# Kernel optimization log

Hardware: AMD Instinct MI355X
Metric: run time of the kernel (lower is better)

## Reference

```python
import jax, jax.numpy as jnp
import numpy as np

B, S, D = 1, 2048, 1024
F = 1408            # expert intermediate dim
E = 16              # num experts
K = 2               # top_k
CAP_FACTOR = 1.25


def _mlp(h, wg, wu, wd):
    # DeepSeek-style gated MLP (SwiGLU, no bias)
    return (jax.nn.silu(h @ wg) * (h @ wu)) @ wd


def setup_inputs() -> dict:
    key = jax.random.key(0)
    ks = jax.random.split(key, 10)
    sd = 0.02
    return {
        "x": jax.random.normal(ks[0], (B, S, D), jnp.float32),
        "router_w": jax.random.normal(ks[1], (D, E), jnp.float32) * sd,
        "router_b": jnp.zeros((E,), jnp.float32),
        "w_gate": jax.random.normal(ks[2], (E, D, F), jnp.float32) * sd,
        "w_up": jax.random.normal(ks[3], (E, D, F), jnp.float32) * sd,
        "w_down": jax.random.normal(ks[4], (E, F, D), jnp.float32) * sd,
        "sw_gate": jax.random.normal(ks[5], (D, F), jnp.float32) * sd,
        "sw_up": jax.random.normal(ks[6], (D, F), jnp.float32) * sd,
        "sw_down": jax.random.normal(ks[7], (F, D), jnp.float32) * sd,
    }


def reference(x, router_w, router_b, w_gate, w_up, w_down, sw_gate, sw_up, sw_down):
    b, s, d = x.shape
    N = b * s
    NK = N * K
    C = int(np.ceil(CAP_FACTOR * NK / E))  # per-expert capacity

    x_tokens = x.reshape(N, d)

    # Router: softmax -> top-k -> renormalize
    logits = x_tokens @ router_w + router_b           # [N, E]
    probs = jax.nn.softmax(logits, axis=-1)
    vals, idx = jax.lax.top_k(probs, K)               # [N, K]
    vals = vals / (jnp.sum(vals, axis=-1, keepdims=True) + 1e-9)
    idx_flat = idx.reshape(NK)                        # int expert ids
    vals_flat = vals.reshape(NK)

    # Position within each expert's buffer = rank in flattened (token, k) order.
    # Same math as (cumsum(one_hot)*one_hot).sum(-1)-1 in the original.
    oh_e = jax.nn.one_hot(idx_flat, E, dtype=x.dtype)             # [NK, E] (small)
    pos = (jnp.cumsum(oh_e, axis=0) * oh_e).sum(axis=1) - 1       # [NK]
    within = (pos < C).astype(x.dtype)                            # capacity mask
    pos_c = jnp.clip(pos, 0, C - 1).astype(jnp.int32)

    # Dispatch: scatter tokens into per-expert buffers. Positions are unique
    # per expert, so scatter-add equals the dense one-hot einsum exactly.
    token_ids = jnp.arange(NK) // K
    x_pair = x_tokens[token_ids] * within[:, None]                # [NK, D]
    expert_inputs = jnp.zeros((E, C, d), x.dtype).at[idx_flat, pos_c].add(x_pair)

    # Grouped expert MLPs
    expert_outputs = jax.vmap(_mlp)(expert_inputs, w_gate, w_up, w_down)  # [E, C, D]

    # Combine: gather back and weight by renormalized router probs
    gathered = expert_outputs[idx_flat, pos_c] * (vals_flat * within)[:, None]
    output_tokens = gathered.reshape(N, K, d).sum(axis=1)         # [N, D]

    return x + _mlp(x, sw_gate, sw_up, sw_down) + output_tokens.reshape(b, s, d)
```

## Files before the change

### kernel.cpp

```cpp
#include <hip/hip_runtime.h>
#include <hip/hip_bf16.h>

#define TOKENS 2048
#define DIM    1024
#define FDIM   1408
#define NEXP   16
#define NK     (TOKENS * 2)
#define CAP    320
#define RPAD   384

typedef __attribute__((ext_vector_type(4))) float f32x4;
typedef __attribute__((ext_vector_type(2))) float f32x2;
typedef __attribute__((ext_vector_type(8))) short s16x8;
typedef __attribute__((ext_vector_type(4))) short s16x4;

__device__ __forceinline__ short f2bf(float f) {
    unsigned int u = __float_as_uint(f);
    u += 0x7FFFu + ((u >> 16) & 1u);
    return (short)(u >> 16);
}
__device__ __forceinline__ float bf2f(short s) {
    return __uint_as_float(((unsigned int)(unsigned short)s) << 16);
}
__device__ __forceinline__ unsigned int f2bf_pk(float lo, float hi) {
    union { __hip_bfloat162 h; unsigned int u; } c;
    c.h = __float22bfloat162_rn(make_float2(lo, hi));
    return c.u;
}

#define GLDS16(gp, lp) __builtin_amdgcn_global_load_lds(                     \
    (const __attribute__((address_space(1))) unsigned int*)(gp),             \
    (__attribute__((address_space(3))) unsigned int*)(lp), 16, 0, 0)

struct GSegF {
    const short* A; long aStride; int aRpad;
    const float* B0; const float* B1; long bStride;
    short* Out; long oStride; int oRpad;
    const int* cnt; int Mb, Nb, N, K, nblocks;
};
struct GSegB {
    const short* A; long aStride; int aRpad;
    const short* B0; long bStride;
    short* Out; long oStride;
    const int* cnt; int Mb, Nb, N, K, nblocks;
};
struct WSeg { const float* in; short* out; int K, N, mats, nblocks; };

__device__ void wchunk_dev(const WSeg& W, int bid)
{
    const int spm = W.K >> 3;
    const int mat = bid / spm, s = bid % spm;
    const float* in  = W.in  + (size_t)mat * W.K * W.N + (size_t)s * 8 * W.N;
    short* out = W.out + (size_t)mat * W.K * W.N + (size_t)s * W.N * 8;
    const int t = threadIdx.x;
    const int iters = (W.N + 511) >> 9;
    for (int it = 0; it < iters; it++) {
        const int n = it * 512 + 2 * t;
        if (n >= W.N) break;
        const float* src = in + n;
        s16x8 o0, o1;
#pragma unroll
        for (int j = 0; j < 8; j++) {
            float2 v = *(const float2*)(src + (size_t)j * W.N);
            o0[j] = f2bf(v.x);
            o1[j] = f2bf(v.y);
        }
        *(s16x8*)(out + (size_t)n * 8)     = o0;
        *(s16x8*)(out + (size_t)n * 8 + 8) = o1;
    }
}

__device__ void router_dev(const float* __restrict__ x, const float* __restrict__ rw,
                           const float* __restrict__ rb, int* __restrict__ idx_flat,
                           float* __restrict__ vals_flat, int bid)
{
    __shared__ float lg[16][17];
    const int t  = threadIdx.x;
    const int tl = t >> 4;
    const int e  = t & 15;
    const int token = bid * 16 + tl;
    const float* xr = x + (size_t)token * DIM;

    float acc = 0.f;
    for (int d4 = 0; d4 < DIM / 4; d4++) {
        float4 xv = *(const float4*)(xr + d4 * 4);
        acc += xv.x * rw[(d4 * 4 + 0) * NEXP + e];
        acc += xv.y * rw[(d4 * 4 + 1) * NEXP + e];
        acc += xv.z * rw[(d4 * 4 + 2) * NEXP + e];
        acc += xv.w * rw[(d4 * 4 + 3) * NEXP + e];
    }
    lg[tl][e] = acc + rb[e];
    __syncthreads();

    if (t < 16) {
        float l[16];
#pragma unroll
        for (int j = 0; j < 16; j++) l[j] = lg[t][j];
        float m = l[0];
#pragma unroll
        for (int j = 1; j < 16; j++) m = fmaxf(m, l[j]);
        float p[16], den = 0.f;
#pragma unroll
        for (int j = 0; j < 16; j++) { p[j] = __expf(l[j] - m); den += p[j]; }
        int i1 = -1; float b1 = -1e30f;
#pragma unroll
        for (int j = 0; j < 16; j++) if (p[j] > b1) { b1 = p[j]; i1 = j; }
        int i2 = -1; float b2 = -1e30f;
#pragma unroll
        for (int j = 0; j < 16; j++) if (j != i1 && p[j] > b2) { b2 = p[j]; i2 = j; }
        float v1 = b1 / den, v2 = b2 / den;
        float s = v1 + v2 + 1e-9f;
        int tok = bid * 16 + t;
        idx_flat[tok * 2 + 0] = i1;
        idx_flat[tok * 2 + 1] = i2;
        vals_flat[tok * 2 + 0] = v1 / s;
        vals_flat[tok * 2 + 1] = v2 / s;
    }
}

__device__ void xconv_dev(const float* __restrict__ x, short* __restrict__ xb, int bid)
{
    const int token = bid * 2 + (threadIdx.x >> 7);
    const int c = threadIdx.x & 127;
    const float* src = x + (size_t)token * DIM + c * 8;
    float4 v0 = *(const float4*)(src);
    float4 v1 = *(const float4*)(src + 4);
    s16x8 o;
    o[0] = f2bf(v0.x); o[1] = f2bf(v0.y); o[2] = f2bf(v0.z); o[3] = f2bf(v0.w);
    o[4] = f2bf(v1.x); o[5] = f2bf(v1.y); o[6] = f2bf(v1.z); o[7] = f2bf(v1.w);
    *(s16x8*)(xb + (size_t)c * (TOKENS * 8) + (size_t)token * 8) = o;
}

__global__ __launch_bounds__(256) void rx_kernel(
    const float* __restrict__ x, const float* __restrict__ rw,
    const float* __restrict__ rb, int* __restrict__ idx_flat,
    float* __restrict__ vals, short* __restrict__ xb)
{
    int bid = blockIdx.x;
    if (bid < TOKENS / 16) { router_dev(x, rw, rb, idx_flat, vals, bid); return; }
    xconv_dev(x, xb, bid - TOKENS / 16);
}

__global__ void scan_kernel(const int* __restrict__ idx_flat,
                            const float* __restrict__ vals,
                            int* __restrict__ dst, float* __restrict__ wgt,
                            int* __restrict__ cnt)
{
    const int lane = threadIdx.x;
    int base[16];
#pragma unroll
    for (int e = 0; e < 16; e++) base[e] = 0;

    for (int c = 0; c < NK / 64; c++) {
        int i = c * 64 + lane;
        int e = idx_flat[i];
        unsigned long long m[16];
#pragma unroll
        for (int ee = 0; ee < 16; ee++) m[ee] = __ballot(e == ee);
        unsigned long long mym = 0ULL; int myb = 0;
#pragma unroll
        for (int ee = 0; ee < 16; ee++) {
            bool sel = (e == ee);
            mym = sel ? m[ee] : mym;
            myb = sel ? base[ee] : myb;
        }
        int pos = myb + (int)__popcll(mym & ((1ULL << lane) - 1ULL));
        bool within = pos < CAP;
        dst[i] = within ? (e * RPAD + pos) : -1;
        wgt[i] = within ? vals[i] : 0.f;
#pragma unroll
        for (int ee = 0; ee < 16; ee++) base[ee] += (int)__popcll(m[ee]);
    }
    if (lane < 16) cnt[lane] = base[lane] < CAP ? base[lane] : CAP;
}

__global__ __launch_bounds__(256) void scatter_kernel(
    const float* __restrict__ x, const int* __restrict__ dst,
    const int* __restrict__ idx_flat, short* __restrict__ ex)
{
    const int i = blockIdx.x * 2 + (threadIdx.x >> 7);
    const int d0 = dst[i];
    if (d0 < 0) return;
    const int e = idx_flat[i];
    const int pos = d0 - e * RPAD;
    const int token = i >> 1;
    const int c = threadIdx.x & 127;
    const float* src = x + (size_t)token * DIM + c * 8;
    float4 v0 = *(const float4*)(src);
    float4 v1 = *(const float4*)(src + 4);
    s16x8 o;
    o[0] = f2bf(v0.x); o[1] = f2bf(v0.y); o[2] = f2bf(v0.z); o[3] = f2bf(v0.w);
    o[4] = f2bf(v1.x); o[5] = f2bf(v1.y); o[6] = f2bf(v1.z); o[7] = f2bf(v1.w);
    *(s16x8*)(ex + (size_t)e * (DIM * RPAD) + (size_t)c * (RPAD * 8) +
              (size_t)pos * 8) = o;
}

template <int NMAT>
__device__ void gemm_fused_dev(const GSegF& S, int bid)
{
    constexpr int BUFS = 4096 * (1 + NMAT);
    __shared__ short lds[2 * BUFS];

    const int cpx = S.nblocks >> 3;
    const int lid = (bid & 7) * cpx + (bid >> 3);
    const int mb  = lid % S.Mb;
    const int t1  = lid / S.Mb;
    const int nb  = t1 % S.Nb;
    const int g   = t1 / S.Nb;
    const int m0 = mb * 128, n0 = nb * 128;
    if (S.cnt != nullptr && m0 >= S.cnt[g]) return;

    const int tid = threadIdx.x, lane = tid & 63, w = tid >> 6;
    const int wr = w >> 1, wc = w & 1, ln = lane & 15, kg = lane >> 4;
    const int N = S.N, K = S.K;

    const short* Ag  = S.A  + (size_t)g * S.aStride + (size_t)m0 * 8;
    const float* Bg0 = S.B0 + (size_t)g * S.bStride + n0;
    const float* Bg1 = nullptr;
    if constexpr (NMAT == 2) Bg1 = S.B1 + (size_t)g * S.bStride + n0;

    const size_t aR8 = (size_t)S.aRpad * 8;

    const int srow = tid & 127, sslab = tid >> 7;
    const short* aS0 = Ag + sslab * aR8 + srow * 8;
    const short* aS1 = Ag + (2 + sslab) * aR8 + srow * 8;
    const int dA0 = w * 512, dA1 = 2048 + w * 512;

    const float* bSrc;
    int rB, cW;
    if constexpr (NMAT == 2) {
        const int c4 = tid & 31, gq = (tid >> 5) & 3, mat = tid >> 7;
        bSrc = (mat ? Bg1 : Bg0) + (size_t)gq * 8 * N + c4 * 4;
        rB = 4096 + mat * 4096 + gq * 1024;
        cW = c4;
    } else {
        const int c2 = tid & 63, gq = tid >> 6;
        bSrc = Bg0 + (size_t)gq * 8 * N + c2 * 2;
        rB = 4096 + gq * 1024;
        cW = c2;
    }

    f32x4 bq[8];
    f32x2 bd[8];

    auto LOADB = [&](int ks) {
        const float* p = bSrc + (size_t)ks * 32 * N;
        if constexpr (NMAT == 2) {
#pragma unroll
            for (int j = 0; j < 8; j++) bq[j] = *(const f32x4*)(p + (size_t)j * N);
        } else {
#pragma unroll
            for (int j = 0; j < 8; j++) bd[j] = *(const f32x2*)(p + (size_t)j * N);
        }
    };
    auto STGA = [&](int buf, int ks) {
        const size_t ka = (size_t)ks * 4 * aR8;
        short* base = lds + buf * BUFS;
        GLDS16(aS0 + ka, base + dA0);
        GLDS16(aS1 + ka, base + dA1);
    };
    auto WRITEB = [&](int buf) {
        short* d = lds + buf * BUFS + rB;
        if constexpr (NMAT == 2) {
#pragma unroll
            for (int j = 0; j < 4; j++) {
                const int colS = (cW * 4 + j) ^ ((cW >> 1) & 7);
                uint4 o;
                o.x = f2bf_pk(bq[0][j], bq[1][j]);
                o.y = f2bf_pk(bq[2][j], bq[3][j]);
                o.z = f2bf_pk(bq[4][j], bq[5][j]);
                o.w = f2bf_pk(bq[6][j], bq[7][j]);
                *(uint4*)(d + colS * 8) = o;
            }
        } else {
#pragma unroll
            for (int j = 0; j < 2; j++) {
                const int colS = (cW * 2 + j) ^ ((cW >> 2) & 7);
                uint4 o;
                o.x = f2bf_pk(bd[0][j], bd[1][j]);
                o.y = f2bf_pk(bd[2][j], bd[3][j]);
                o.z = f2bf_pk(bd[4][j], bd[5][j]);
                o.w = f2bf_pk(bd[6][j], bd[7][j]);
                *(uint4*)(d + colS * 8) = o;
            }
        }
    };

    const int aO = kg * 1024 + (wr * 64 + ln) * 8;

    f32x4 acc[NMAT][4][4] = {};
    const int nt = K / 32;

    LOADB(0);
    __builtin_amdgcn_sched_barrier(0);
    STGA(0, 0);
    __builtin_amdgcn_sched_barrier(0);
    WRITEB(0);
    __builtin_amdgcn_sched_barrier(0);
    LOADB(1);
    __builtin_amdgcn_sched_barrier(0);
    asm volatile("s_waitcnt lgkmcnt(0)" ::: "memory");
    STGA(1, 1);
    __builtin_amdgcn_sched_barrier(0);

    int cur = 0;
    for (int ks = 0; ks < nt; ks++) {
        if (ks + 1 < nt) asm volatile("s_waitcnt vmcnt(10)" ::: "memory");
        else             asm volatile("s_waitcnt vmcnt(0)"  ::: "memory");
        __builtin_amdgcn_s_barrier();
        __builtin_amdgcn_sched_barrier(0);

        const short* base = lds + cur * BUFS;
        s16x8 af[4];
#pragma unroll
        for (int m = 0; m < 4; m++)
            af[m] = *(const s16x8*)(base + aO + m * 128);
        s16x8 bf[NMAT][4];
#pragma unroll
        for (int nf = 0; nf < 4; nf++) {
            const int col  = wc * 64 + nf * 16 + ln;
            const int colS = col ^ ((col >> 3) & 7);
#pragma unroll
            for (int mat = 0; mat < NMAT; mat++)
                bf[mat][nf] = *(const s16x8*)(base + 4096 + mat * 4096 +
                                              kg * 1024 + colS * 8);
        }

#pragma unroll
        for (int nf = 0; nf < 4; nf++)
#pragma unroll
            for (int m = 0; m < 4; m++)
#pragma unroll
                for (int mat = 0; mat < NMAT; mat++)
                    acc[mat][m][nf] = __builtin_amdgcn_mfma_f32_16x16x32_bf16(
                        af[m], bf[mat][nf], acc[mat][m][nf], 0, 0, 0);

        if (ks + 1 < nt) WRITEB(cur ^ 1);

        __builtin_amdgcn_sched_barrier(0);
        if (ks + 2 < nt) LOADB(ks + 2);
        __builtin_amdgcn_sched_barrier(0);
        asm volatile("s_waitcnt lgkmcnt(0)" ::: "memory");
        __builtin_amdgcn_s_barrier();

        if (ks + 2 < nt) {
            STGA(cur, ks + 2);
            __builtin_amdgcn_sched_barrier(0);
        }
        cur ^= 1;
    }

#pragma unroll
    for (int m = 0; m < 4; m++) {
#pragma unroll
        for (int nf = 0; nf < 4; nf++) {
            const int row = m0 + wr * 64 + m * 16 + kg * 4;
            const int col = n0 + wc * 64 + nf * 16 + ln;
#pragma unroll
            for (int j = 0; j < 4; j++) {
                if constexpr (NMAT == 2) {
                    float gv = acc[0][m][nf][j];
                    float uv = acc[1][m][nf][j];
                    float v = gv / (1.f + __expf(-gv)) * uv;
                    S.Out[(size_t)g * S.oStride + (size_t)(col >> 3) * (S.oRpad * 8) +
                          (size_t)(row + j) * 8 + (col & 7)] = f2bf(v);
                } else {
                    S.Out[(size_t)g * S.oStride + (size_t)(row + j) * N + col] =
                        f2bf(acc[0][m][nf][j]);
                }
            }
        }
    }
}

__device__ void gemm_down_dev(const GSegB& S, int bid)
{
    constexpr int BUFS = 10240;
    __shared__ short lds[2 * BUFS];

    const int cpx = S.nblocks >> 3;
    const int lid = (bid & 7) * cpx + (bid >> 3);
    const int mb  = lid % S.Mb;
    const int t1  = lid / S.Mb;
    const int nb  = t1 % S.Nb;
    const int g   = t1 / S.Nb;
    const int m0 = mb * 64, n0 = nb * 256;
    if (S.cnt != nullptr && m0 >= S.cnt[g]) return;

    const int tid = threadIdx.x, lane = tid & 63, w = tid >> 6;
    const int wr = w >> 1, wc = w & 1, ln = lane & 15, kg = lane >> 4;
    const int N = S.N, K = S.K;

    const short* Ag = S.A  + (size_t)g * S.aStride + (size_t)m0 * 8;
    const short* Bg = S.B0 + (size_t)g * S.bStride + (size_t)n0 * 8;

    const size_t aR8 = (size_t)S.aRpad * 8;
    const size_t n8  = (size_t)N * 8;

    const short* aS = Ag + (size_t)(tid >> 6) * aR8 + (size_t)(tid & 63) * 8;
    const short* bS = Bg + (size_t)tid * 8;
    const int dA = w * 512;

    auto STG = [&](int buf, int ks) {
        const size_t ka = (size_t)ks * 4 * aR8;
        const size_t kb = (size_t)ks * 4 * n8;
        short* base = lds + buf * BUFS;
        GLDS16(aS + ka, base + dA);
#pragma unroll
        for (int i = 0; i < 4; i++)
            GLDS16(bS + kb + (size_t)i * n8, base + 2048 + i * 2048 + w * 512);
    };

    const int aO = kg * 512 + (wr * 32 + ln) * 8;
    const int bBase = 2048 + kg * 2048 + (wc * 128 + ln) * 8;

    f32x4 acc[2][8] = {};
    const int nt = K / 32;
    STG(0, 0); STG(1, 1);
    int cur = 0;
    for (int ks = 0; ks < nt; ks++) {
        if (ks + 1 < nt) asm volatile("s_waitcnt vmcnt(5)" ::: "memory");
        else             asm volatile("s_waitcnt vmcnt(0)" ::: "memory");
        __builtin_amdgcn_s_barrier();
        __builtin_amdgcn_sched_barrier(0);

        const short* base = lds + cur * BUFS;
        s16x8 af[2];
        af[0] = *(const s16x8*)(base + aO);
        af[1] = *(const s16x8*)(base + aO + 128);
        s16x8 bf[8];
#pragma unroll
        for (int nf = 0; nf < 8; nf++)
            bf[nf] = *(const s16x8*)(base + bBase + nf * 128);

#pragma unroll
        for (int nf = 0; nf < 8; nf++)
#pragma unroll
            for (int m = 0; m < 2; m++)
                acc[m][nf] = __builtin_amdgcn_mfma_f32_16x16x32_bf16(
                    af[m], bf[nf], acc[m][nf], 0, 0, 0);

        __builtin_amdgcn_sched_barrier(0);
        __builtin_amdgcn_s_barrier();
        if (ks + 2 < nt) STG(cur, ks + 2);
        cur ^= 1;
    }

#pragma unroll
    for (int m = 0; m < 2; m++) {
#pragma unroll
        for (int nf = 0; nf < 8; nf++) {
            const int row = m0 + wr * 32 + m * 16 + kg * 4;
            const int col = n0 + wc * 128 + nf * 16 + ln;
#pragma unroll
            for (int j = 0; j < 4; j++)
                S.Out[(size_t)g * S.oStride + (size_t)(row + j) * N + col] =
                    f2bf(acc[m][nf][j]);
        }
    }
}

__global__ __launch_bounds__(256, 2) void gateup_kernel(GSegF s0, GSegF s1,
                                                        WSeg w0, WSeg w1)
{
    int bid = blockIdx.x;
    if (bid < s0.nblocks) { gemm_fused_dev<2>(s0, bid); return; }
    bid -= s0.nblocks;
    if (bid < s1.nblocks) { gemm_fused_dev<2>(s1, bid); return; }
    bid -= s1.nblocks;
    if (bid < w0.nblocks) { wchunk_dev(w0, bid); return; }
    wchunk_dev(w1, bid - w0.nblocks);
}

__global__ __launch_bounds__(256, 3) void down_kernel(GSegB s0, GSegB s1)
{
    int bid = blockIdx.x;
    if (bid < s0.nblocks) { gemm_down_dev(s0, bid); return; }
    gemm_down_dev(s1, bid - s0.nblocks);
}

__global__ __launch_bounds__(256) void combine_kernel(
    const float* __restrict__ x, const short* __restrict__ shout,
    const short* __restrict__ eout, const int* __restrict__ dst,
    const float* __restrict__ wgt, float* __restrict__ out)
{
    const int t = blockIdx.x;
    const int d = threadIdx.x * 4;
    size_t o = (size_t)t * DIM + d;
    float4 xv = *(const float4*)(x + o);
    s16x4 sv = *(const s16x4*)(shout + o);
    float r0 = xv.x + bf2f(sv[0]);
    float r1 = xv.y + bf2f(sv[1]);
    float r2 = xv.z + bf2f(sv[2]);
    float r3 = xv.w + bf2f(sv[3]);
#pragma unroll
    for (int k = 0; k < 2; k++) {
        int di = dst[t * 2 + k];
        if (di >= 0) {
            float wv = wgt[t * 2 + k];
            s16x4 ev = *(const s16x4*)(eout + (size_t)di * DIM + d);
            r0 += wv * bf2f(ev[0]);
            r1 += wv * bf2f(ev[1]);
            r2 += wv * bf2f(ev[2]);
            r3 += wv * bf2f(ev[3]);
        }
    }
    float4 rv = {r0, r1, r2, r3};
    *(float4*)(out + o) = rv;
}

extern "C" void kernel_launch(void* const* d_in, const int* in_sizes, int n_in,
                              void* d_out, int out_size, void* d_ws, size_t ws_size,
                              hipStream_t stream)
{
    const float* x   = (const float*)d_in[0];
    const float* rw  = (const float*)d_in[1];
    const float* rb  = (const float*)d_in[2];
    const float* wg  = (const float*)d_in[3];
    const float* wu  = (const float*)d_in[4];
    const float* wd  = (const float*)d_in[5];
    const float* swg = (const float*)d_in[6];
    const float* swu = (const float*)d_in[7];
    const float* swd = (const float*)d_in[8];
    float* out = (float*)d_out;

    char* wp = (char*)d_ws;
    auto alloc = [&](size_t b) { char* p = wp; wp += (b + 255) & ~(size_t)255; return p; };
    int*   idx_flat = (int*)alloc((size_t)NK * 4);
    float* vals     = (float*)alloc((size_t)NK * 4);
    int*   dst      = (int*)alloc((size_t)NK * 4);
    float* wgt      = (float*)alloc((size_t)NK * 4);
    int*   cnt      = (int*)alloc(64);
    short* xb       = (short*)alloc((size_t)TOKENS * DIM * 2);
    short* ex       = (short*)alloc((size_t)NEXP * RPAD * DIM * 2);
    short* acte     = (short*)alloc((size_t)NEXP * RPAD * FDIM * 2);
    short* acts     = (short*)alloc((size_t)TOKENS * FDIM * 2);
    short* eout     = (short*)alloc((size_t)NEXP * RPAD * DIM * 2);
    short* shout    = (short*)alloc((size_t)TOKENS * DIM * 2);
    short* wdC      = (short*)alloc((size_t)NEXP * DIM * FDIM * 2);
    short* swdC     = (short*)alloc((size_t)DIM * FDIM * 2);

    rx_kernel<<<TOKENS / 16 + TOKENS / 2, 256, 0, stream>>>(x, rw, rb,
                                                            idx_flat, vals, xb);
    scan_kernel<<<1, 64, 0, stream>>>(idx_flat, vals, dst, wgt, cnt);

    scatter_kernel<<<NK / 2, 256, 0, stream>>>(x, dst, idx_flat, ex);

    GSegF segGE = {ex, (long)RPAD * DIM, RPAD, wg, wu, (long)DIM * FDIM,
                   acte, (long)RPAD * FDIM, RPAD, cnt, 3, 11, FDIM, DIM, 3 * 11 * NEXP};
    GSegF segGS = {xb, 0L, TOKENS, swg, swu, 0L,
                   acts, 0L, TOKENS, nullptr, 16, 11, FDIM, DIM, 16 * 11};
    WSeg Wd  = {wd,  wdC,  FDIM, DIM, NEXP, NEXP * (FDIM / 8)};
    WSeg Wsd = {swd, swdC, FDIM, DIM, 1,    FDIM / 8};
    gateup_kernel<<<segGE.nblocks + segGS.nblocks + Wd.nblocks + Wsd.nblocks,
                    256, 0, stream>>>(segGE, segGS, Wd, Wsd);

    GSegB segDE = {acte, (long)RPAD * FDIM, RPAD, wdC, (long)DIM * FDIM,
                   eout, (long)RPAD * DIM, cnt, 6, 4, DIM, FDIM, 6 * 4 * NEXP};
    GSegB segDS = {acts, 0L, TOKENS, swdC, 0L,
                   shout, 0L, nullptr, 32, 4, DIM, FDIM, 32 * 4};
    down_kernel<<<segDE.nblocks + segDS.nblocks, 256, 0, stream>>>(segDE, segDS);

    combine_kernel<<<TOKENS, 256, 0, stream>>>(x, shout, eout, dst, wgt, out);
}
```

Before: 224.1 us.

## Enlarge gate/up GEMM tile to 256 rows with 512-thread blocks

Reworks the fused gate/up GEMM to compute 256x128 output tiles with 512 threads (8 waves) instead of 128x128 with 256 threads. Each fp32 weight tile converted to bf16 in LDS is then reused across twice as many rows, halving per-token weight traffic and conversion work. Expert capacity padding (384) now spans two 256-row tiles, so the expert buffer is over-allocated and output rows are clipped against a row limit. The trade-off is fewer blocks, higher LDS and register use per block, and wasted compute on padded rows; the weight-conversion loop is also adjusted for the larger block.

```diff
diff --git a/kernel.cpp b/kernel.cpp
--- a/kernel.cpp
+++ b/kernel.cpp
@@ -36,7 +36,7 @@
     const short* A; long aStride; int aRpad;
     const float* B0; const float* B1; long bStride;
     short* Out; long oStride; int oRpad;
-    const int* cnt; int Mb, Nb, N, K, nblocks;
+    const int* cnt; int Mb, Nb, N, K, rlim, nblocks;
 };
 struct GSegB {
     const short* A; long aStride; int aRpad;
@@ -53,10 +53,7 @@
     const float* in  = W.in  + (size_t)mat * W.K * W.N + (size_t)s * 8 * W.N;
     short* out = W.out + (size_t)mat * W.K * W.N + (size_t)s * W.N * 8;
     const int t = threadIdx.x;
-    const int iters = (W.N + 511) >> 9;
-    for (int it = 0; it < iters; it++) {
-        const int n = it * 512 + 2 * t;
-        if (n >= W.N) break;
+    for (int n = 2 * t; n < W.N; n += 1024) {
         const float* src = in + n;
         s16x8 o0, o1;
 #pragma unroll
@@ -195,10 +192,9 @@
               (size_t)pos * 8) = o;
 }
 
-template <int NMAT>
-__device__ void gemm_fused_dev(const GSegF& S, int bid)
-{
-    constexpr int BUFS = 4096 * (1 + NMAT);
+__device__ void gemm_fused256_dev(const GSegF& S, int bid)
+{
+    constexpr int BUFS = 8192 + 8192;
     __shared__ short lds[2 * BUFS];
 
     const int cpx = S.nblocks >> 3;
@@ -207,7 +203,7 @@
     const int t1  = lid / S.Mb;
     const int nb  = t1 % S.Nb;
     const int g   = t1 / S.Nb;
-    const int m0 = mb * 128, n0 = nb * 128;
+    const int m0 = mb * 256, n0 = nb * 128;
     if (S.cnt != nullptr && m0 >= S.cnt[g]) return;
 
     const int tid = threadIdx.x, lane = tid & 63, w = tid >> 6;
@@ -216,42 +212,28 @@
 
     const short* Ag  = S.A  + (size_t)g * S.aStride + (size_t)m0 * 8;
     const float* Bg0 = S.B0 + (size_t)g * S.bStride + n0;
-    const float* Bg1 = nullptr;
-    if constexpr (NMAT == 2) Bg1 = S.B1 + (size_t)g * S.bStride + n0;
+    const float* Bg1 = S.B1 + (size_t)g * S.bStride + n0;
 
     const size_t aR8 = (size_t)S.aRpad * 8;
 
-    const int srow = tid & 127, sslab = tid >> 7;
-    const short* aS0 = Ag + sslab * aR8 + srow * 8;
-    const short* aS1 = Ag + (2 + sslab) * aR8 + srow * 8;
-    const int dA0 = w * 512, dA1 = 2048 + w * 512;
-
-    const float* bSrc;
-    int rB, cW;
-    if constexpr (NMAT == 2) {
-        const int c4 = tid & 31, gq = (tid >> 5) & 3, mat = tid >> 7;
-        bSrc = (mat ? Bg1 : Bg0) + (size_t)gq * 8 * N + c4 * 4;
-        rB = 4096 + mat * 4096 + gq * 1024;
-        cW = c4;
-    } else {
-        const int c2 = tid & 63, gq = tid >> 6;
-        bSrc = Bg0 + (size_t)gq * 8 * N + c2 * 2;
-        rB = 4096 + gq * 1024;
-        cW = c2;
-    }
-
-    f32x4 bq[8];
-    f32x2 bd[8];
+    const short* aS0 = Ag + (size_t)(tid >> 8) * aR8 + (size_t)(tid & 255) * 8;
+    const short* aS1 = Ag + (size_t)(2 + (tid >> 8)) * aR8 + (size_t)(tid & 255) * 8;
+    const int dA0 = w * 512, dA1 = 4096 + w * 512;
+
+    const int matid = tid >> 8, r = tid & 255;
+    const int c4 = (r & 31) * 4;
+    const int g4 = r >> 5;
+    const float* bSrc = (matid ? Bg1 : Bg0) + (size_t)g4 * 4 * N + c4;
+    const int bKg  = g4 >> 1;
+    const int bOff = (g4 & 1) * 4;
+    const int rB = 8192 + matid * 4096 + bKg * 1024;
+
+    f32x4 bq[4];
 
     auto LOADB = [&](int ks) {
         const float* p = bSrc + (size_t)ks * 32 * N;
-        if constexpr (NMAT == 2) {
-#pragma unroll
-            for (int j = 0; j < 8; j++) bq[j] = *(const f32x4*)(p + (size_t)j * N);
-        } else {
-#pragma unroll
-            for (int j = 0; j < 8; j++) bd[j] = *(const f32x2*)(p + (size_t)j * N);
-        }
+#pragma unroll
+        for (int j = 0; j < 4; j++) bq[j] = *(const f32x4*)(p + (size_t)j * N);
     };
     auto STGA = [&](int buf, int ks) {
         const size_t ka = (size_t)ks * 4 * aR8;
@@ -260,35 +242,21 @@
         GLDS16(aS1 + ka, base + dA1);
     };
     auto WRITEB = [&](int buf) {
-        short* d = lds + buf * BUFS + rB;
-        if constexpr (NMAT == 2) {
-#pragma unroll
-            for (int j = 0; j < 4; j++) {
-                const int colS = (cW * 4 + j) ^ ((cW >> 1) & 7);
-                uint4 o;
-                o.x = f2bf_pk(bq[0][j], bq[1][j]);
-                o.y = f2bf_pk(bq[2][j], bq[3][j]);
-                o.z = f2bf_pk(bq[4][j], bq[5][j]);
-                o.w = f2bf_pk(bq[6][j], bq[7][j]);
-                *(uint4*)(d + colS * 8) = o;
-            }
-        } else {
-#pragma unroll
-            for (int j = 0; j < 2; j++) {
-                const int colS = (cW * 2 + j) ^ ((cW >> 2) & 7);
-                uint4 o;
-                o.x = f2bf_pk(bd[0][j], bd[1][j]);
-                o.y = f2bf_pk(bd[2][j], bd[3][j]);
-                o.z = f2bf_pk(bd[4][j], bd[5][j]);
-                o.w = f2bf_pk(bd[6][j], bd[7][j]);
-                *(uint4*)(d + colS * 8) = o;
-            }
+        short* d = lds + buf * BUFS + rB + bOff;
+#pragma unroll
+        for (int j = 0; j < 4; j++) {
+            const int col = c4 + j;
+            const int colS = col ^ ((col >> 3) & 7);
+            s16x4 o;
+            o[0] = f2bf(bq[0][j]); o[1] = f2bf(bq[1][j]);
+            o[2] = f2bf(bq[2][j]); o[3] = f2bf(bq[3][j]);
+            *(s16x4*)(d + colS * 8) = o;
         }
     };
 
-    const int aO = kg * 1024 + (wr * 64 + ln) * 8;
-
-    f32x4 acc[NMAT][4][4] = {};
+    const int aO = kg * 2048 + (wr * 64 + ln) * 8;
+
+    f32x4 acc[2][4][4] = {};
     const int nt = K / 32;
 
     LOADB(0);
@@ -305,8 +273,8 @@
 
     int cur = 0;
     for (int ks = 0; ks < nt; ks++) {
-        if (ks + 1 < nt) asm volatile("s_waitcnt vmcnt(10)" ::: "memory");
-        else             asm volatile("s_waitcnt vmcnt(0)"  ::: "memory");
+        if (ks + 1 < nt) asm volatile("s_waitcnt vmcnt(6)" ::: "memory");
+        else             asm volatile("s_waitcnt vmcnt(0)" ::: "memory");
         __builtin_amdgcn_s_barrier();
         __builtin_amdgcn_sched_barrier(0);
 
@@ -315,14 +283,14 @@
 #pragma unroll
         for (int m = 0; m < 4; m++)
             af[m] = *(const s16x8*)(base + aO + m * 128);
-        s16x8 bf[NMAT][4];
+        s16x8 bf[2][4];
 #pragma unroll
         for (int nf = 0; nf < 4; nf++) {
             const int col  = wc * 64 + nf * 16 + ln;
             const int colS = col ^ ((col >> 3) & 7);
 #pragma unroll
-            for (int mat = 0; mat < NMAT; mat++)
-                bf[mat][nf] = *(const s16x8*)(base + 4096 + mat * 4096 +
+            for (int mat = 0; mat < 2; mat++)
+                bf[mat][nf] = *(const s16x8*)(base + 8192 + mat * 4096 +
                                               kg * 1024 + colS * 8);
         }
 
@@ -331,7 +299,7 @@
 #pragma unroll
             for (int m = 0; m < 4; m++)
 #pragma unroll
-                for (int mat = 0; mat < NMAT; mat++)
+                for (int mat = 0; mat < 2; mat++)
                     acc[mat][m][nf] = __builtin_amdgcn_mfma_f32_16x16x32_bf16(
                         af[m], bf[mat][nf], acc[mat][m][nf], 0, 0, 0);
 
@@ -356,17 +324,14 @@
         for (int nf = 0; nf < 4; nf++) {
             const int row = m0 + wr * 64 + m * 16 + kg * 4;
             const int col = n0 + wc * 64 + nf * 16 + ln;
-#pragma unroll
-            for (int j = 0; j < 4; j++) {
-                if constexpr (NMAT == 2) {
+            if (row < S.rlim) {
+#pragma unroll
+                for (int j = 0; j < 4; j++) {
                     float gv = acc[0][m][nf][j];
                     float uv = acc[1][m][nf][j];
                     float v = gv / (1.f + __expf(-gv)) * uv;
                     S.Out[(size_t)g * S.oStride + (size_t)(col >> 3) * (S.oRpad * 8) +
                           (size_t)(row + j) * 8 + (col & 7)] = f2bf(v);
-                } else {
-                    S.Out[(size_t)g * S.oStride + (size_t)(row + j) * N + col] =
-                        f2bf(acc[0][m][nf][j]);
                 }
             }
         }
@@ -460,13 +425,13 @@
     }
 }
 
-__global__ __launch_bounds__(256, 2) void gateup_kernel(GSegF s0, GSegF s1,
+__global__ __launch_bounds__(512, 2) void gateup_kernel(GSegF s0, GSegF s1,
                                                         WSeg w0, WSeg w1)
 {
     int bid = blockIdx.x;
-    if (bid < s0.nblocks) { gemm_fused_dev<2>(s0, bid); return; }
+    if (bid < s0.nblocks) { gemm_fused256_dev(s0, bid); return; }
     bid -= s0.nblocks;
-    if (bid < s1.nblocks) { gemm_fused_dev<2>(s1, bid); return; }
+    if (bid < s1.nblocks) { gemm_fused256_dev(s1, bid); return; }
     bid -= s1.nblocks;
     if (bid < w0.nblocks) { wchunk_dev(w0, bid); return; }
     wchunk_dev(w1, bid - w0.nblocks);
@@ -532,7 +497,7 @@
     float* wgt      = (float*)alloc((size_t)NK * 4);
     int*   cnt      = (int*)alloc(64);
     short* xb       = (short*)alloc((size_t)TOKENS * DIM * 2);
-    short* ex       = (short*)alloc((size_t)NEXP * RPAD * DIM * 2);
+    short* ex       = (short*)alloc(((size_t)NEXP * RPAD + 128) * DIM * 2);
     short* acte     = (short*)alloc((size_t)NEXP * RPAD * FDIM * 2);
     short* acts     = (short*)alloc((size_t)TOKENS * FDIM * 2);
     short* eout     = (short*)alloc((size_t)NEXP * RPAD * DIM * 2);
@@ -547,13 +512,15 @@
     scatter_kernel<<<NK / 2, 256, 0, stream>>>(x, dst, idx_flat, ex);
 
     GSegF segGE = {ex, (long)RPAD * DIM, RPAD, wg, wu, (long)DIM * FDIM,
-                   acte, (long)RPAD * FDIM, RPAD, cnt, 3, 11, FDIM, DIM, 3 * 11 * NEXP};
+                   acte, (long)RPAD * FDIM, RPAD, cnt, 2, 11, FDIM, DIM,
+                   RPAD, 2 * 11 * NEXP};
     GSegF segGS = {xb, 0L, TOKENS, swg, swu, 0L,
-                   acts, 0L, TOKENS, nullptr, 16, 11, FDIM, DIM, 16 * 11};
+                   acts, 0L, TOKENS, nullptr, 8, 11, FDIM, DIM,
+                   TOKENS, 8 * 11};
     WSeg Wd  = {wd,  wdC,  FDIM, DIM, NEXP, NEXP * (FDIM / 8)};
     WSeg Wsd = {swd, swdC, FDIM, DIM, 1,    FDIM / 8};
     gateup_kernel<<<segGE.nblocks + segGS.nblocks + Wd.nblocks + Wsd.nblocks,
-                    256, 0, stream>>>(segGE, segGS, Wd, Wsd);
+                    512, 0, stream>>>(segGE, segGS, Wd, Wsd);
 
     GSegB segDE = {acte, (long)RPAD * FDIM, RPAD, wdC, (long)DIM * FDIM,
                    eout, (long)RPAD * DIM, cnt, 6, 4, DIM, FDIM, 6 * 4 * NEXP};
```

Measured after the change: 236.6 us. 5.6% more time.
